# Kernel tuning notes

Hardware: AMD Instinct MI355X
Metric: run time of the kernel (lower is better)

The kernel has to match this reference:

```python
import jax, jax.numpy as jnp
import numpy as np

B, NK, NQ = 16, 1024, 1024
D_IN, D_V, D_H = 3, 8, 128
NUGGET = 1e-3   # diagonal regularizer for the kriging covariance solve
EPS = 1e-12     # keeps sqrt differentiable at zero distance


def _mlp(x, w1, b1, w2, b2, w3, b3):
    # Linear -> ReLU -> Linear -> ReLU -> Linear (torch Linear: y = x @ W.T + b)
    h = jax.nn.relu(x @ w1.T + b1)
    h = jax.nn.relu(h @ w2.T + b2)
    return h @ w3.T + b3


def _cdist(a, b):
    # a: [B,N,D], b: [B,M,D] -> [B,N,M] Euclidean distances
    d2 = (jnp.sum(a * a, -1)[:, :, None]
          + jnp.sum(b * b, -1)[:, None, :]
          - 2.0 * jnp.einsum('bnd,bmd->bnm', a, b))
    return jnp.sqrt(jnp.maximum(d2, 0.0) + EPS)


def _linear_init(key, out_f, in_f):
    k1, k2 = jax.random.split(key)
    lim = 1.0 / np.sqrt(in_f)
    w = jax.random.uniform(k1, (out_f, in_f), jnp.float32, -lim, lim)
    b = jax.random.uniform(k2, (out_f,), jnp.float32, -lim, lim)
    return w, b


def setup_inputs() -> dict:
    key = jax.random.key(0)
    ks = jax.random.split(key, 10)
    KEY = jax.random.normal(ks[0], (B, NK, D_IN), jnp.float32)
    VALUE = jax.random.normal(ks[1], (B, NK, D_V), jnp.float32)
    QUERY = jax.random.normal(ks[2], (B, NQ, D_IN), jnp.float32)
    W1_w, W1_b = _linear_init(ks[3], D_H, D_IN)
    W2_w, W2_b = _linear_init(ks[4], D_H, D_H)
    W3_w, W3_b = _linear_init(ks[5], D_IN, D_H)
    Wv1_w, Wv1_b = _linear_init(ks[6], D_H, D_V)
    Wv2_w, Wv2_b = _linear_init(ks[7], D_H, D_H)
    Wv3_w, Wv3_b = _linear_init(ks[8], D_V, D_H)
    return dict(KEY=KEY, VALUE=VALUE, QUERY=QUERY,
                W1_w=W1_w, W1_b=W1_b, W2_w=W2_w, W2_b=W2_b, W3_w=W3_w, W3_b=W3_b,
                Wv1_w=Wv1_w, Wv1_b=Wv1_b, Wv2_w=Wv2_w, Wv2_b=Wv2_b, Wv3_w=Wv3_w, Wv3_b=Wv3_b)


def reference(KEY, VALUE, QUERY,
              W1_w, W1_b, W2_w, W2_b, W3_w, W3_b,
              Wv1_w, Wv1_b, Wv2_w, Wv2_b, Wv3_w, Wv3_b):
    # shared MLP on KEY and QUERY, separate MLP on VALUE
    Wk = _mlp(KEY, W1_w, W1_b, W2_w, W2_b, W3_w, W3_b)
    Wq = _mlp(QUERY, W1_w, W1_b, W2_w, W2_b, W3_w, W3_b)
    Wv = _mlp(VALUE, Wv1_w, Wv1_b, Wv2_w, Wv2_b, Wv3_w, Wv3_b)
    VALUE_scale = VALUE * Wv                  # einsum('bij,bij->bij')
    # kriging prediction with learned elementwise coordinate scalings
    Ks = KEY * Wk                             # [B,NK,D_IN]
    Qs = QUERY * Wq                           # [B,NQ,D_IN]
    C_kk = jnp.exp(-_cdist(Ks, Ks)) + NUGGET * jnp.eye(NK, dtype=KEY.dtype)  # [B,NK,NK]
    C_qk = jnp.exp(-_cdist(Qs, Ks))                                          # [B,NQ,NK]
    # kriging weights: solve C_kk @ lam = C_qk^T  -> lam [B,NK,NQ]
    lam = jnp.linalg.solve(C_kk, jnp.swapaxes(C_qk, 1, 2))
    # prediction: weighted sum of scaled values -> [B,NQ,D_V]
    return jnp.einsum('bkq,bkv->bqv', lam, VALUE_scale)
```

## Files before the change

### kernel.cpp

```cpp
#include <hip/hip_runtime.h>
#include <hip/hip_bf16.h>


__device__ __forceinline__ int row_of(int e) {
    int i = (int)((sqrtf(8.0f * (float)e + 1.0f) - 1.0f) * 0.5f);
    while ((i + 1) * (i + 2) / 2 <= e) i++;
    while (i * (i + 1) / 2 > e) i--;
    return i;
}

__global__ void k_transpose(const float* __restrict__ W2, const float* __restrict__ Wv2,
                            float* __restrict__ W2T, float* __restrict__ Wv2T) {
    int tid = blockIdx.x * 256 + threadIdx.x;
    int e = tid & 16383;
    int r = e >> 7, c = e & 127;
    if (tid < 16384) W2T[c * 128 + r] = W2[e];
    else             Wv2T[c * 128 + r] = Wv2[e];
}

template<int DI, int P>
__device__ __forceinline__ void mlp_body(const float* __restrict__ in,
                                         float* __restrict__ out, int base,
                                         const float* __restrict__ W1,
                                         const float* __restrict__ b1,
                                         const float* __restrict__ W2T,
                                         const float* __restrict__ b2,
                                         const float* __restrict__ W3,
                                         const float* __restrict__ b3) {
    __shared__ float xs[P][DI];
    __shared__ float h1[P][128];
    __shared__ float h2[P][129];
    int t = threadIdx.x;
    for (int i = t; i < P * DI; i += 128) xs[i / DI][i % DI] = in[base * DI + i];
    __syncthreads();
    float w1r[DI];
#pragma unroll
    for (int d = 0; d < DI; d++) w1r[d] = W1[t * DI + d];
    float b1t = b1[t], b2t = b2[t];
#pragma unroll
    for (int p = 0; p < P; p++) {
        float s = b1t;
#pragma unroll
        for (int d = 0; d < DI; d++) s += w1r[d] * xs[p][d];
        h1[p][t] = fmaxf(s, 0.0f);
    }
    __syncthreads();
    float acc[P];
#pragma unroll
    for (int p = 0; p < P; p++) acc[p] = b2t;
    for (int k = 0; k < 128; k++) {
        float w = W2T[k * 128 + t];
#pragma unroll
        for (int p = 0; p < P; p++) acc[p] += w * h1[p][k];
    }
#pragma unroll
    for (int p = 0; p < P; p++) h2[p][t] = fmaxf(acc[p], 0.0f);
    __syncthreads();
    if (t < P * DI) {
        int p = t / DI, d = t % DI;
        float s = b3[d];
        for (int k = 0; k < 128; k++) s += W3[d * 128 + k] * h2[p][k];
        int gi = base * DI + t;
        out[gi] = in[gi] * s;
    }
}

__global__ void k_mlp_kq(const float* __restrict__ KEY, float* __restrict__ Ks,
                         const float* __restrict__ QUERY, float* __restrict__ Qs,
                         const float* __restrict__ W1, const float* __restrict__ b1,
                         const float* __restrict__ W2T, const float* __restrict__ b2,
                         const float* __restrict__ W3, const float* __restrict__ b3) {
    if (blockIdx.x < 512)
        mlp_body<3, 32>(KEY, Ks, blockIdx.x * 32, W1, b1, W2T, b2, W3, b3);
    else
        mlp_body<3, 32>(QUERY, Qs, (blockIdx.x - 512) * 32, W1, b1, W2T, b2, W3, b3);
}

__global__ void k_mlp_v(const float* __restrict__ VALUE, float* __restrict__ Vs,
                        const float* __restrict__ W1, const float* __restrict__ b1,
                        const float* __restrict__ W2T, const float* __restrict__ b2,
                        const float* __restrict__ W3, const float* __restrict__ b3) {
    mlp_body<8, 16>(VALUE, Vs, blockIdx.x * 16, W1, b1, W2T, b2, W3, b3);
}

__global__ void k_buildC(const float* __restrict__ Ks, float* __restrict__ C) {
    long idx = (long)blockIdx.x * 256 + threadIdx.x;
    int b = (int)(idx >> 20);
    int rem = (int)(idx & 1048575);
    int i = rem >> 10, j = rem & 1023;
    const float* a = Ks + ((long)b * 1024 + i) * 3;
    const float* bb = Ks + ((long)b * 1024 + j) * 3;
    float d0 = a[0] - bb[0], d1 = a[1] - bb[1], d2 = a[2] - bb[2];
    float dist = sqrtf(d0 * d0 + d1 * d1 + d2 * d2 + 1e-12f);
    float v = __expf(-dist);
    if (i == j) v += 1e-3f;
    C[idx] = v;
}

__device__ void potf_body(float* __restrict__ C, float* __restrict__ V,
                          int o, int last, int b) {
    int tid = threadIdx.x;
    float* A = C + (long)b * 1048576;
    float* Vp = V + (long)b * 8192;
    __shared__ float T[128][132];
    __shared__ __align__(16) float cv[128][8];
    __shared__ __align__(16) float cw[128][8];
    __shared__ __align__(16) float Pn[128][8];
    __shared__ __align__(16) float St[32][132];
    __shared__ float rsd[128];
    __shared__ float W[32][33];
    __shared__ float zs[128][9];
    bool active = (tid < 136);
    int ti = 0, tj = 0;
    if (active) { ti = row_of(tid); tj = tid - ti * (ti + 1) / 2; }
    int r0 = ti * 8, c0t = tj * 8;
    float Treg[8][8];
    if (active) {
        const float* src = A + (long)(o + r0) * 1024 + o + c0t;
#pragma unroll
        for (int i = 0; i < 8; i++) {
            float4 va = *(const float4*)(src + (long)i * 1024);
            float4 vb = *(const float4*)(src + (long)i * 1024 + 4);
            Treg[i][0] = va.x; Treg[i][1] = va.y; Treg[i][2] = va.z; Treg[i][3] = va.w;
            Treg[i][4] = vb.x; Treg[i][5] = vb.y; Treg[i][6] = vb.z; Treg[i][7] = vb.w;
        }
    }
    int lane = tid & 63;
    __syncthreads();
    if (o > 0) {
        for (int kc = 0; kc < 4; kc++) {
            {
                int r = tid >> 1, lk = (tid & 1) * 16;
                const float* sp = A + (long)(o + r) * 1024 + (o - 128) + kc * 32 + lk;
#pragma unroll
                for (int k4 = 0; k4 < 4; k4++) {
                    float4 v = *(const float4*)(sp + 4 * k4);
                    St[lk + 4*k4    ][r] = v.x;
                    St[lk + 4*k4 + 1][r] = v.y;
                    St[lk + 4*k4 + 2][r] = v.z;
                    St[lk + 4*k4 + 3][r] = v.w;
                }
            }
            __syncthreads();
            if (active) {
#pragma unroll 4
                for (int k = 0; k < 32; k++) {
                    float4 a0 = *(const float4*)&St[k][r0];
                    float4 a1 = *(const float4*)&St[k][r0 + 4];
                    float4 b0 = *(const float4*)&St[k][c0t];
                    float4 b1 = *(const float4*)&St[k][c0t + 4];
                    float aa[8] = {a0.x,a0.y,a0.z,a0.w,a1.x,a1.y,a1.z,a1.w};
                    float bb[8] = {b0.x,b0.y,b0.z,b0.w,b1.x,b1.y,b1.z,b1.w};
#pragma unroll
                    for (int i = 0; i < 8; i++)
#pragma unroll
                        for (int j = 0; j < 8; j++) Treg[i][j] -= aa[i] * bb[j];
                }
            }
            __syncthreads();
        }
    }
    for (int jbt = 0; jbt < 16; jbt++) {
        int jb = jbt * 8;
        if (active && tj == jbt) {
#pragma unroll
            for (int i = 0; i < 8; i++) {
                *(float4*)&Pn[r0 + i][0] = make_float4(Treg[i][0], Treg[i][1], Treg[i][2], Treg[i][3]);
                *(float4*)&Pn[r0 + i][4] = make_float4(Treg[i][4], Treg[i][5], Treg[i][6], Treg[i][7]);
            }
        }
        __syncthreads();
        if (tid < 64) {
            int r1 = lane, r2 = 64 + lane;
            float v1[8], v2[8], w1[8], w2[8];
#pragma unroll
            for (int q = 0; q < 8; q++) {
                int j = jb + q;
                int jl = j & 63;
                bool hi = (j >= 64);
                float a1 = Pn[r1][q], a2 = Pn[r2][q];
#pragma unroll
                for (int p = 0; p < 8; p++) {
                    if (p < q) {
                        float wj = __shfl(hi ? w2[p] : w1[p], jl);
                        a1 -= v1[p] * wj;
                        a2 -= v2[p] * wj;
                    }
                }
                v1[q] = a1; v2[q] = a2;
                float dj = __shfl(hi ? a2 : a1, jl);
                float dinv = 1.0f / dj;
                w1[q] = a1 * dinv; w2[q] = a2 * dinv;
            }
            *(float4*)&cv[r1][0] = make_float4(v1[0], v1[1], v1[2], v1[3]);
            *(float4*)&cv[r1][4] = make_float4(v1[4], v1[5], v1[6], v1[7]);
            *(float4*)&cv[r2][0] = make_float4(v2[0], v2[1], v2[2], v2[3]);
            *(float4*)&cv[r2][4] = make_float4(v2[4], v2[5], v2[6], v2[7]);
            *(float4*)&cw[r1][0] = make_float4(w1[0], w1[1], w1[2], w1[3]);
            *(float4*)&cw[r1][4] = make_float4(w1[4], w1[5], w1[6], w1[7]);
            *(float4*)&cw[r2][0] = make_float4(w2[0], w2[1], w2[2], w2[3]);
            *(float4*)&cw[r2][4] = make_float4(w2[4], w2[5], w2[6], w2[7]);
        }
        __syncthreads();
        if (active && tj == jbt) {
#pragma unroll
            for (int i = 0; i < 8; i++) {
                float4 va = *(const float4*)&cv[r0 + i][0];
                float4 vb = *(const float4*)&cv[r0 + i][4];
                Treg[i][0] = va.x; Treg[i][1] = va.y; Treg[i][2] = va.z; Treg[i][3] = va.w;
                Treg[i][4] = vb.x; Treg[i][5] = vb.y; Treg[i][6] = vb.z; Treg[i][7] = vb.w;
            }
        } else if (active && tj > jbt) {
#pragma unroll
            for (int h = 0; h < 2; h++) {
                float va4[8][4], wb4[8][4];
#pragma unroll
                for (int i = 0; i < 8; i++) {
                    float4 v = *(const float4*)&cv[r0 + i][h * 4];
                    va4[i][0] = v.x; va4[i][1] = v.y; va4[i][2] = v.z; va4[i][3] = v.w;
                }
#pragma unroll
                for (int j = 0; j < 8; j++) {
                    float4 v = *(const float4*)&cw[c0t + j][h * 4];
                    wb4[j][0] = v.x; wb4[j][1] = v.y; wb4[j][2] = v.z; wb4[j][3] = v.w;
                }
#pragma unroll
                for (int i = 0; i < 8; i++)
#pragma unroll
                    for (int j = 0; j < 8; j++)
                        Treg[i][j] -= va4[i][0] * wb4[j][0] + va4[i][1] * wb4[j][1]
                                    + va4[i][2] * wb4[j][2] + va4[i][3] * wb4[j][3];
            }
        }
        __syncthreads();
    }
    if (active) {
#pragma unroll
        for (int i = 0; i < 8; i++) {
            *(float4*)&T[r0 + i][c0t]     = make_float4(Treg[i][0], Treg[i][1], Treg[i][2], Treg[i][3]);
            *(float4*)&T[r0 + i][c0t + 4] = make_float4(Treg[i][4], Treg[i][5], Treg[i][6], Treg[i][7]);
        }
    }
    __syncthreads();
    int rg = tid >> 4;
    int cg = tid & 15;
    int wv = tid >> 6;
    if (tid < 128) rsd[tid] = rsqrtf(T[tid][tid]);
    __syncthreads();
#pragma unroll
    for (int j = 0; j < 8; j++) {
        int c = cg + 16 * j;
#pragma unroll
        for (int i = 0; i < 8; i++) {
            int r = rg * 8 + i;
            if (c <= r) T[r][c] *= rsd[c];
            else        T[r][c] = 0.0f;
        }
    }
    __syncthreads();
    if (lane < 32) {
        int d0 = wv * 32;
        int j = lane;
        float x[32];
#pragma unroll
        for (int i = 0; i < 32; i++) {
            float dinv = 1.0f / T[d0 + i][d0 + i];
            float s = 0.0f;
#pragma unroll
            for (int k = 0; k < i; k++) s += T[d0 + i][d0 + k] * x[k];
            x[i] = (i == j) ? dinv : -s * dinv;
        }
#pragma unroll
        for (int i = 0; i < 32; i++) T[d0 + i][d0 + j] = x[i];
    }
    __syncthreads();
    int orr = tid >> 3;
    int oc = (tid & 7) * 4;
    for (int j = 0; j < 3; j++) {
        for (int i = j + 1; i < 4; i++) {
            float w0 = 0, w1 = 0, w2 = 0, w3 = 0;
            for (int kb = j; kb < i; kb++) {
#pragma unroll 8
                for (int kk = 0; kk < 32; kk++) {
                    float l = T[i * 32 + orr][kb * 32 + kk];
                    w0 += l * T[kb * 32 + kk][j * 32 + oc    ];
                    w1 += l * T[kb * 32 + kk][j * 32 + oc + 1];
                    w2 += l * T[kb * 32 + kk][j * 32 + oc + 2];
                    w3 += l * T[kb * 32 + kk][j * 32 + oc + 3];
                }
            }
            W[orr][oc] = w0; W[orr][oc+1] = w1; W[orr][oc+2] = w2; W[orr][oc+3] = w3;
            __syncthreads();
            float v0 = 0, v1 = 0, v2 = 0, v3 = 0;
#pragma unroll 8
            for (int kk = 0; kk < 32; kk++) {
                float l = T[i * 32 + orr][i * 32 + kk];
                v0 += l * W[kk][oc    ];
                v1 += l * W[kk][oc + 1];
                v2 += l * W[kk][oc + 2];
                v3 += l * W[kk][oc + 3];
            }
            __syncthreads();
            T[i * 32 + orr][j * 32 + oc    ] = -v0;
            T[i * 32 + orr][j * 32 + oc + 1] = -v1;
            T[i * 32 + orr][j * 32 + oc + 2] = -v2;
            T[i * 32 + orr][j * 32 + oc + 3] = -v3;
            __syncthreads();
        }
    }
    {
        int r = tid >> 1, c0 = (tid & 1) * 64;
        float* dst = A + (long)(o + r) * 1024 + o + c0;
#pragma unroll
        for (int k = 0; k < 16; k++) {
            int c = c0 + 4 * k;
            float4 v = make_float4(T[r][c], T[r][c + 1], T[r][c + 2], T[r][c + 3]);
            *(float4*)(dst + 4 * k) = v;
        }
    }
    {
        int k = tid >> 1, c0 = (tid & 1) * 4;
        float4 v = *(const float4*)&Vp[(o + k) * 8 + c0];
        zs[k][c0] = v.x; zs[k][c0 + 1] = v.y; zs[k][c0 + 2] = v.z; zs[k][c0 + 3] = v.w;
    }
    __syncthreads();
    {
        int r = tid & 127, c0 = (tid >> 7) * 4;
        float y0 = 0, y1 = 0, y2 = 0, y3 = 0;
#pragma unroll 8
        for (int k = 0; k < 128; k++) {
            float l = T[r][k];
            y0 += l * zs[k][c0    ];
            y1 += l * zs[k][c0 + 1];
            y2 += l * zs[k][c0 + 2];
            y3 += l * zs[k][c0 + 3];
        }
        if (!last) {
            *(float4*)&Vp[(o + r) * 8 + c0] = make_float4(y0, y1, y2, y3);
        } else {
            __syncthreads();
            zs[r][c0] = y0; zs[r][c0+1] = y1; zs[r][c0+2] = y2; zs[r][c0+3] = y3;
            __syncthreads();
            float x0 = 0, x1 = 0, x2 = 0, x3 = 0;
#pragma unroll 8
            for (int k = 0; k < 128; k++) {
                float l = T[k][r];
                x0 += l * zs[k][c0    ];
                x1 += l * zs[k][c0 + 1];
                x2 += l * zs[k][c0 + 2];
                x3 += l * zs[k][c0 + 3];
            }
            *(float4*)&Vp[(o + r) * 8 + c0] = make_float4(x0, x1, x2, x3);
        }
    }
}

__device__ void syrk_body(float* __restrict__ C, int o, int pti, int ptj, int b) {
    float* A = C + (long)b * 1048576;
    int bi = o + 128 + pti * 128, bj = o + 128 + ptj * 128;
    __shared__ float As[32][132];
    __shared__ float Bs[32][132];
    int tid = threadIdx.x;
    int tx = tid & 15, ty = tid >> 4;
    float acc[8][8] = {};
    int lr = tid >> 1;
    int lk = (tid & 1) * 16;
    bool diag = (bi == bj);
    for (int kc = 0; kc < 128; kc += 32) {
        {
            const float* src = A + (long)(bi + lr) * 1024 + o + kc + lk;
#pragma unroll
            for (int k4 = 0; k4 < 4; k4++) {
                float4 v = *(const float4*)(src + 4 * k4);
                As[lk + 4*k4    ][lr] = v.x;
                As[lk + 4*k4 + 1][lr] = v.y;
                As[lk + 4*k4 + 2][lr] = v.z;
                As[lk + 4*k4 + 3][lr] = v.w;
            }
            if (!diag) {
                const float* sb = A + (long)(bj + lr) * 1024 + o + kc + lk;
#pragma unroll
                for (int k4 = 0; k4 < 4; k4++) {
                    float4 v = *(const float4*)(sb + 4 * k4);
                    Bs[lk + 4*k4    ][lr] = v.x;
                    Bs[lk + 4*k4 + 1][lr] = v.y;
                    Bs[lk + 4*k4 + 2][lr] = v.z;
                    Bs[lk + 4*k4 + 3][lr] = v.w;
                }
            }
        }
        __syncthreads();
        {
            const float (*Bp)[132] = diag ? As : Bs;
#pragma unroll
            for (int k = 0; k < 32; k++) {
                float4 a0 = *(const float4*)&As[k][ty * 8];
                float4 a1 = *(const float4*)&As[k][ty * 8 + 4];
                float4 b0 = *(const float4*)&Bp[k][tx * 8];
                float4 b1 = *(const float4*)&Bp[k][tx * 8 + 4];
                float aa[8] = {a0.x,a0.y,a0.z,a0.w,a1.x,a1.y,a1.z,a1.w};
                float bb[8] = {b0.x,b0.y,b0.z,b0.w,b1.x,b1.y,b1.z,b1.w};
#pragma unroll
                for (int i = 0; i < 8; i++)
#pragma unroll
                    for (int j = 0; j < 8; j++) acc[i][j] += aa[i] * bb[j];
            }
        }
        __syncthreads();
    }
#pragma unroll
    for (int i = 0; i < 8; i++) {
        int r = bi + ty * 8 + i;
        float* dst = A + (long)r * 1024 + bj + tx * 8;
        if (!diag) {
            float4 p0 = *(const float4*)dst;
            float4 p1 = *(const float4*)(dst + 4);
            p0.x -= acc[i][0]; p0.y -= acc[i][1]; p0.z -= acc[i][2]; p0.w -= acc[i][3];
            p1.x -= acc[i][4]; p1.y -= acc[i][5]; p1.z -= acc[i][6]; p1.w -= acc[i][7];
            *(float4*)dst = p0;
            *(float4*)(dst + 4) = p1;
        } else {
#pragma unroll
            for (int j = 0; j < 8; j++) {
                int c = bj + tx * 8 + j;
                if (c <= r) dst[j] -= acc[i][j];
            }
        }
    }
}

__global__ __launch_bounds__(256) void k_potf_syrk(float* __restrict__ C,
                                                   float* __restrict__ V,
                                                   int o, int last) {
    int bx = blockIdx.x;
    if (bx < 16) {
        potf_body(C, V, o, last, bx);
    } else {
        int v = bx - 16;
        int bb = v & 15;
        int p = (v >> 4) + 1;
        int tii = row_of(p);
        int tjj = p - tii * (tii + 1) / 2;
        syrk_body(C, o - 128, tii, tjj, bb);
    }
}

__global__ __launch_bounds__(256) void k_trsmg(float* __restrict__ C,
                                               float* __restrict__ V, int o) {
    int b = blockIdx.y;
    float* A = C + (long)b * 1048576;
    float* Vp = V + (long)b * 8192;
    int bi = o + 128 + blockIdx.x * 128;
    const float* Linv = A + (long)o * 1024 + o;
    __shared__ float As[32][132];
    __shared__ float Ls[32][132];
    int tid = threadIdx.x;
    int tx = tid & 15, ty = tid >> 4;
    float acc[8][8] = {};
    int lr = tid >> 1;
    int lk = (tid & 1) * 16;
    for (int kc = 0; kc < 128; kc += 32) {
        const float* src = A + (long)(bi + lr) * 1024 + o + kc + lk;
        const float* sl  = Linv + (long)lr * 1024 + kc + lk;
#pragma unroll
        for (int k4 = 0; k4 < 4; k4++) {
            float4 v = *(const float4*)(src + 4 * k4);
            As[lk + 4*k4    ][lr] = v.x;
            As[lk + 4*k4 + 1][lr] = v.y;
            As[lk + 4*k4 + 2][lr] = v.z;
            As[lk + 4*k4 + 3][lr] = v.w;
            float4 w = *(const float4*)(sl + 4 * k4);
            Ls[lk + 4*k4    ][lr] = w.x;
            Ls[lk + 4*k4 + 1][lr] = w.y;
            Ls[lk + 4*k4 + 2][lr] = w.z;
            Ls[lk + 4*k4 + 3][lr] = w.w;
        }
        __syncthreads();
#pragma unroll
        for (int k = 0; k < 32; k++) {
            float4 a0 = *(const float4*)&As[k][ty * 8];
            float4 a1 = *(const float4*)&As[k][ty * 8 + 4];
            float4 b0 = *(const float4*)&Ls[k][tx * 8];
            float4 b1 = *(const float4*)&Ls[k][tx * 8 + 4];
            float aa[8] = {a0.x,a0.y,a0.z,a0.w,a1.x,a1.y,a1.z,a1.w};
            float bb[8] = {b0.x,b0.y,b0.z,b0.w,b1.x,b1.y,b1.z,b1.w};
#pragma unroll
            for (int i = 0; i < 8; i++)
#pragma unroll
                for (int j = 0; j < 8; j++) acc[i][j] += aa[i] * bb[j];
        }
        __syncthreads();
    }
#pragma unroll
    for (int i = 0; i < 8; i++) {
        float* dst = A + (long)(bi + ty * 8 + i) * 1024 + o + tx * 8;
        *(float4*)dst       = make_float4(acc[i][0], acc[i][1], acc[i][2], acc[i][3]);
        *(float4*)(dst + 4) = make_float4(acc[i][4], acc[i][5], acc[i][6], acc[i][7]);
    }
    float* ysf = &Ls[0][0];
    {
        int k = tid >> 1, c0 = (tid & 1) * 4;
        float4 v = *(const float4*)&Vp[(o + k) * 8 + c0];
        ysf[k * 9 + c0] = v.x; ysf[k * 9 + c0 + 1] = v.y;
        ysf[k * 9 + c0 + 2] = v.z; ysf[k * 9 + c0 + 3] = v.w;
    }
    __syncthreads();
    float zacc0 = 0, zacc1 = 0, zacc2 = 0, zacc3 = 0;
    int zr = tid & 127, zc0 = (tid >> 7) * 4;
#pragma unroll
    for (int ch = 0; ch < 4; ch++) {
        if ((tx >> 2) == ch) {
            int cb = (tx & 3) * 8;
#pragma unroll
            for (int j = 0; j < 8; j++)
#pragma unroll
                for (int i = 0; i < 8; i++)
                    As[cb + j][ty * 8 + i] = acc[i][j];
        }
        __syncthreads();
#pragma unroll 8
        for (int k = 0; k < 32; k++) {
            float l = As[k][zr];
            const float* yp = &ysf[(ch * 32 + k) * 9 + zc0];
            zacc0 += l * yp[0]; zacc1 += l * yp[1];
            zacc2 += l * yp[2]; zacc3 += l * yp[3];
        }
        __syncthreads();
    }
    float* vp = &Vp[(bi + zr) * 8 + zc0];
    float4 old = *(const float4*)vp;
    old.x -= zacc0; old.y -= zacc1; old.z -= zacc2; old.w -= zacc3;
    *(float4*)vp = old;
}

__global__ __launch_bounds__(256) void k_bstep(const float* __restrict__ C,
                                               float* __restrict__ V, int k) {
    int b = blockIdx.y, j = blockIdx.x, tid = threadIdx.x;
    const float* A = C + (long)b * 1048576;
    float* Vp = V + (long)b * 8192;
    __shared__ float Lb[128][129];
    __shared__ float xs[128][9];
    __shared__ float ys[128][9];
    {
        int kk = tid >> 1, c0 = (tid & 1) * 4;
        float4 v = *(const float4*)&Vp[(k * 128 + kk) * 8 + c0];
        xs[kk][c0] = v.x; xs[kk][c0+1] = v.y; xs[kk][c0+2] = v.z; xs[kk][c0+3] = v.w;
    }
#pragma unroll
    for (int m = 0; m < 16; m++) {
        int e = tid + m * 256;
        int i = e >> 5, j4 = (e & 31) * 4;
        float4 v = *(const float4*)&A[(long)(k * 128 + i) * 1024 + j * 128 + j4];
        Lb[i][j4] = v.x; Lb[i][j4+1] = v.y; Lb[i][j4+2] = v.z; Lb[i][j4+3] = v.w;
    }
    __syncthreads();
    int r = tid & 127, c0 = (tid >> 7) * 4;
    float u0 = 0, u1 = 0, u2 = 0, u3 = 0;
#pragma unroll 8
    for (int kk = 0; kk < 128; kk++) {
        float l = Lb[kk][r];
        u0 += l * xs[kk][c0    ];
        u1 += l * xs[kk][c0 + 1];
        u2 += l * xs[kk][c0 + 2];
        u3 += l * xs[kk][c0 + 3];
    }
    float* vp = &Vp[(j * 128 + r) * 8 + c0];
    float4 old = *(const float4*)vp;
    old.x -= u0; old.y -= u1; old.z -= u2; old.w -= u3;
    if (j < k - 1) {
        *(float4*)vp = old;
    } else {
        ys[r][c0] = old.x; ys[r][c0+1] = old.y; ys[r][c0+2] = old.z; ys[r][c0+3] = old.w;
        __syncthreads();
        int o = j * 128;
#pragma unroll
        for (int m = 0; m < 16; m++) {
            int e = tid + m * 256;
            int i = e >> 5, j4 = (e & 31) * 4;
            float4 v = *(const float4*)&A[(long)(o + i) * 1024 + o + j4];
            Lb[i][j4] = v.x; Lb[i][j4+1] = v.y; Lb[i][j4+2] = v.z; Lb[i][j4+3] = v.w;
        }
        __syncthreads();
        float x0 = 0, x1 = 0, x2 = 0, x3 = 0;
#pragma unroll 8
        for (int kk = 0; kk < 128; kk++) {
            float l = Lb[kk][r];
            x0 += l * ys[kk][c0    ];
            x1 += l * ys[kk][c0 + 1];
            x2 += l * ys[kk][c0 + 2];
            x3 += l * ys[kk][c0 + 3];
        }
        *(float4*)vp = make_float4(x0, x1, x2, x3);
    }
}

__global__ void k_out(const float* __restrict__ Qs, const float* __restrict__ Ks,
                      const float* __restrict__ X, float* __restrict__ out) {
    int b = blockIdx.x >> 4;
    int qc = blockIdx.x & 15;
    int t = threadIdx.x;
    int q = t & 63, ks = t >> 6;
    __shared__ float kx[1024][3];
    __shared__ __align__(16) float xv[1024][8];
    __shared__ float red[4][64][8];
    for (int i = t; i < 3072; i += 256) kx[i / 3][i % 3] = Ks[b * 3072 + i];
    for (int i = t; i < 8192; i += 256) xv[i >> 3][i & 7] = X[b * 8192 + i];
    __syncthreads();
    int gq = b * 1024 + qc * 64 + q;
    const float* qp = Qs + (long)gq * 3;
    float qx = qp[0], qy = qp[1], qz = qp[2];
    float acc[8] = {};
    int k0 = ks * 256;
#pragma unroll 2
    for (int k = k0; k < k0 + 256; k++) {
        float dx = qx - kx[k][0], dy = qy - kx[k][1], dz = qz - kx[k][2];
        float w = __expf(-sqrtf(dx * dx + dy * dy + dz * dz + 1e-12f));
        float4 xa = *(const float4*)&xv[k][0];
        float4 xb = *(const float4*)&xv[k][4];
        acc[0] += w * xa.x; acc[1] += w * xa.y; acc[2] += w * xa.z; acc[3] += w * xa.w;
        acc[4] += w * xb.x; acc[5] += w * xb.y; acc[6] += w * xb.z; acc[7] += w * xb.w;
    }
#pragma unroll
    for (int c = 0; c < 8; c++) red[ks][q][c] = acc[c];
    __syncthreads();
    if (ks == 0) {
        float* op = out + (long)gq * 8;
#pragma unroll
        for (int c = 0; c < 8; c++)
            op[c] = red[0][q][c] + red[1][q][c] + red[2][q][c] + red[3][q][c];
    }
}

extern "C" void kernel_launch(void* const* d_in, const int* in_sizes, int n_in,
                              void* d_out, int out_size, void* d_ws, size_t ws_size,
                              hipStream_t stream) {
    const float* KEY   = (const float*)d_in[0];
    const float* VALUE = (const float*)d_in[1];
    const float* QUERY = (const float*)d_in[2];
    const float* W1w = (const float*)d_in[3];  const float* W1b = (const float*)d_in[4];
    const float* W2w = (const float*)d_in[5];  const float* W2b = (const float*)d_in[6];
    const float* W3w = (const float*)d_in[7];  const float* W3b = (const float*)d_in[8];
    const float* Wv1w = (const float*)d_in[9]; const float* Wv1b = (const float*)d_in[10];
    const float* Wv2w = (const float*)d_in[11];const float* Wv2b = (const float*)d_in[12];
    const float* Wv3w = (const float*)d_in[13];const float* Wv3b = (const float*)d_in[14];

    float* ws  = (float*)d_ws;
    float* C    = ws;
    float* Ks   = C + 16777216;
    float* Qs   = Ks + 49152;
    float* Vs   = Qs + 49152;
    float* W2T  = Vs + 131072;
    float* Wv2T = W2T + 16384;

    float* out = (float*)d_out;

    hipLaunchKernelGGL(k_transpose, dim3(128), dim3(256), 0, stream, W2w, Wv2w, W2T, Wv2T);
    hipLaunchKernelGGL(k_mlp_kq, dim3(1024), dim3(128), 0, stream,
                       KEY, Ks, QUERY, Qs, W1w, W1b, W2T, W2b, W3w, W3b);
    hipLaunchKernelGGL(k_mlp_v, dim3(1024), dim3(128), 0, stream,
                       VALUE, Vs, Wv1w, Wv1b, Wv2T, Wv2b, Wv3w, Wv3b);
    hipLaunchKernelGGL(k_buildC, dim3(65536), dim3(256), 0, stream, Ks, C);

    for (int s = 0; s < 8; s++) {
        int o = s * 128;
        int np = 0;
        if (s >= 1) { int ntp = 8 - s; np = ntp * (ntp + 1) / 2 - 1; }
        hipLaunchKernelGGL(k_potf_syrk, dim3(16 + np * 16), dim3(256), 0, stream,
                           C, Vs, o, (s == 7) ? 1 : 0);
        int nt = 7 - s;
        if (nt > 0)
            hipLaunchKernelGGL(k_trsmg, dim3(nt, 16), dim3(256), 0, stream, C, Vs, o);
    }
    for (int k = 7; k >= 1; k--)
        hipLaunchKernelGGL(k_bstep, dim3(k, 16), dim3(256), 0, stream, C, Vs, k);

    hipLaunchKernelGGL(k_out, dim3(256), dim3(256), 0, stream, Qs, Ks, Vs, out);
}
```

Measured before the change: 1.140 ms.

## Fuse blocked Cholesky and solve steps into one persistent kernel with per-batch barriers

```diff
diff --git a/kernel.cpp b/kernel.cpp
--- a/kernel.cpp
+++ b/kernel.cpp
@@ -9,9 +9,37 @@
     return i;
 }
 
+struct PotfS {
+    float T[128][132];
+    float cv[128][8];
+    float cw[128][8];
+    float Pn[128][8];
+    float St[32][132];
+    float rsd[128];
+    float W[32][33];
+    float zs[128][9];
+};
+struct SyrkS { float As[32][132]; float Bs[32][132]; };
+struct TrsmS { float As[32][132]; float Ls[32][132]; };
+struct BstepS { float Lb[128][129]; float xs[128][9]; float ys[128][9]; };
+#define SMEM_BYTES 106112
+
+__device__ __forceinline__ void batch_barrier(unsigned int* cnt) {
+    __syncthreads();
+    if (threadIdx.x == 0) {
+        __threadfence();
+        atomicAdd(cnt, 1u);
+        while (atomicAdd(cnt, 0u) < 16u) __builtin_amdgcn_s_sleep(1);
+    }
+    __syncthreads();
+    __threadfence();
+}
+
 __global__ void k_transpose(const float* __restrict__ W2, const float* __restrict__ Wv2,
-                            float* __restrict__ W2T, float* __restrict__ Wv2T) {
+                            float* __restrict__ W2T, float* __restrict__ Wv2T,
+                            unsigned int* __restrict__ bar) {
     int tid = blockIdx.x * 256 + threadIdx.x;
+    if (tid < 512) bar[tid] = 0u;
     int e = tid & 16383;
     int r = e >> 7, c = e & 127;
     if (tid < 16384) W2T[c * 128 + r] = W2[e];
@@ -98,18 +126,19 @@
 }
 
 __device__ void potf_body(float* __restrict__ C, float* __restrict__ V,
-                          int o, int last, int b) {
+                          int o, int last, int b, char* smem) {
+    PotfS& S = *(PotfS*)smem;
+    float (&T)[128][132] = S.T;
+    float (&cv)[128][8] = S.cv;
+    float (&cw)[128][8] = S.cw;
+    float (&Pn)[128][8] = S.Pn;
+    float (&St)[32][132] = S.St;
+    float (&rsd)[128] = S.rsd;
+    float (&W)[32][33] = S.W;
+    float (&zs)[128][9] = S.zs;
     int tid = threadIdx.x;
     float* A = C + (long)b * 1048576;
     float* Vp = V + (long)b * 8192;
-    __shared__ float T[128][132];
-    __shared__ __align__(16) float cv[128][8];
-    __shared__ __align__(16) float cw[128][8];
-    __shared__ __align__(16) float Pn[128][8];
-    __shared__ __align__(16) float St[32][132];
-    __shared__ float rsd[128];
-    __shared__ float W[32][33];
-    __shared__ float zs[128][9];
     bool active = (tid < 136);
     int ti = 0, tj = 0;
     if (active) { ti = row_of(tid); tj = tid - ti * (ti + 1) / 2; }
@@ -355,17 +384,20 @@
     }
 }
 
-__device__ void syrk_body(float* __restrict__ C, int o, int pti, int ptj, int b) {
+__device__ void syrk_body(float* __restrict__ C, int o, int pti, int ptj, int b,
+                          char* smem) {
+    SyrkS& S = *(SyrkS*)smem;
+    float (&As)[32][132] = S.As;
+    float (&Bs)[32][132] = S.Bs;
     float* A = C + (long)b * 1048576;
     int bi = o + 128 + pti * 128, bj = o + 128 + ptj * 128;
-    __shared__ float As[32][132];
-    __shared__ float Bs[32][132];
     int tid = threadIdx.x;
     int tx = tid & 15, ty = tid >> 4;
     float acc[8][8] = {};
     int lr = tid >> 1;
     int lk = (tid & 1) * 16;
     bool diag = (bi == bj);
+    __syncthreads();
     for (int kc = 0; kc < 128; kc += 32) {
         {
             const float* src = A + (long)(bi + lr) * 1024 + o + kc + lk;
@@ -429,36 +461,21 @@
     }
 }
 
-__global__ __launch_bounds__(256) void k_potf_syrk(float* __restrict__ C,
-                                                   float* __restrict__ V,
-                                                   int o, int last) {
-    int bx = blockIdx.x;
-    if (bx < 16) {
-        potf_body(C, V, o, last, bx);
-    } else {
-        int v = bx - 16;
-        int bb = v & 15;
-        int p = (v >> 4) + 1;
-        int tii = row_of(p);
-        int tjj = p - tii * (tii + 1) / 2;
-        syrk_body(C, o - 128, tii, tjj, bb);
-    }
-}
-
-__global__ __launch_bounds__(256) void k_trsmg(float* __restrict__ C,
-                                               float* __restrict__ V, int o) {
-    int b = blockIdx.y;
+__device__ void trsmg_body(float* __restrict__ C, float* __restrict__ V,
+                           int o, int rowblk, int b, char* smem) {
+    TrsmS& S = *(TrsmS*)smem;
+    float (&As)[32][132] = S.As;
+    float (&Ls)[32][132] = S.Ls;
     float* A = C + (long)b * 1048576;
     float* Vp = V + (long)b * 8192;
-    int bi = o + 128 + blockIdx.x * 128;
+    int bi = o + 128 + rowblk * 128;
     const float* Linv = A + (long)o * 1024 + o;
-    __shared__ float As[32][132];
-    __shared__ float Ls[32][132];
     int tid = threadIdx.x;
     int tx = tid & 15, ty = tid >> 4;
     float acc[8][8] = {};
     int lr = tid >> 1;
     int lk = (tid & 1) * 16;
+    __syncthreads();
     for (int kc = 0; kc < 128; kc += 32) {
         const float* src = A + (long)(bi + lr) * 1024 + o + kc + lk;
         const float* sl  = Linv + (long)lr * 1024 + kc + lk;
@@ -533,14 +550,16 @@
     *(float4*)vp = old;
 }
 
-__global__ __launch_bounds__(256) void k_bstep(const float* __restrict__ C,
-                                               float* __restrict__ V, int k) {
-    int b = blockIdx.y, j = blockIdx.x, tid = threadIdx.x;
+__device__ void bstep_body(const float* __restrict__ C, float* __restrict__ V,
+                           int k, int j, int b, char* smem) {
+    BstepS& S = *(BstepS*)smem;
+    float (&Lb)[128][129] = S.Lb;
+    float (&xs)[128][9] = S.xs;
+    float (&ys)[128][9] = S.ys;
     const float* A = C + (long)b * 1048576;
     float* Vp = V + (long)b * 8192;
-    __shared__ float Lb[128][129];
-    __shared__ float xs[128][9];
-    __shared__ float ys[128][9];
+    int tid = threadIdx.x;
+    __syncthreads();
     {
         int kk = tid >> 1, c0 = (tid & 1) * 4;
         float4 v = *(const float4*)&Vp[(k * 128 + kk) * 8 + c0];
@@ -591,6 +610,40 @@
             x3 += l * ys[kk][c0 + 3];
         }
         *(float4*)vp = make_float4(x0, x1, x2, x3);
+    }
+}
+
+__global__ __launch_bounds__(256) void k_chol(float* __restrict__ C,
+                                              float* __restrict__ V,
+                                              unsigned int* __restrict__ bar) {
+    __shared__ __align__(16) char smem[SMEM_BYTES];
+    int b = blockIdx.x & 15;
+    int role = blockIdx.x >> 4;
+    unsigned int* cnt = bar + b * 32;
+    int slot = 0;
+    for (int s = 0; s < 8; s++) {
+        int o = s * 128;
+        if (role == 0) {
+            potf_body(C, V, o, (s == 7) ? 1 : 0, b, smem);
+        } else if (s >= 1) {
+            int ntp = 8 - s;
+            int npt = ntp * (ntp + 1) / 2;
+            for (int p = role; p < npt; p += 15) {
+                int tii = row_of(p);
+                int tjj = p - tii * (tii + 1) / 2;
+                syrk_body(C, o - 128, tii, tjj, b, smem);
+            }
+        }
+        batch_barrier(cnt + slot); slot++;
+        int nt = 7 - s;
+        if (nt > 0) {
+            if (role < nt) trsmg_body(C, V, o, role, b, smem);
+            batch_barrier(cnt + slot); slot++;
+        }
+    }
+    for (int k = 7; k >= 1; k--) {
+        if (role < k) bstep_body(C, V, k, role, b, smem);
+        batch_barrier(cnt + slot); slot++;
     }
 }
 
@@ -651,28 +704,19 @@
     float* Vs   = Qs + 49152;
     float* W2T  = Vs + 131072;
     float* Wv2T = W2T + 16384;
+    unsigned int* bar = (unsigned int*)(Wv2T + 16384);
 
     float* out = (float*)d_out;
 
-    hipLaunchKernelGGL(k_transpose, dim3(128), dim3(256), 0, stream, W2w, Wv2w, W2T, Wv2T);
+    hipLaunchKernelGGL(k_transpose, dim3(128), dim3(256), 0, stream,
+                       W2w, Wv2w, W2T, Wv2T, bar);
     hipLaunchKernelGGL(k_mlp_kq, dim3(1024), dim3(128), 0, stream,
                        KEY, Ks, QUERY, Qs, W1w, W1b, W2T, W2b, W3w, W3b);
     hipLaunchKernelGGL(k_mlp_v, dim3(1024), dim3(128), 0, stream,
                        VALUE, Vs, Wv1w, Wv1b, Wv2T, Wv2b, Wv3w, Wv3b);
     hipLaunchKernelGGL(k_buildC, dim3(65536), dim3(256), 0, stream, Ks, C);
 
-    for (int s = 0; s < 8; s++) {
-        int o = s * 128;
-        int np = 0;
-        if (s >= 1) { int ntp = 8 - s; np = ntp * (ntp + 1) / 2 - 1; }
-        hipLaunchKernelGGL(k_potf_syrk, dim3(16 + np * 16), dim3(256), 0, stream,
-                           C, Vs, o, (s == 7) ? 1 : 0);
-        int nt = 7 - s;
-        if (nt > 0)
-            hipLaunchKernelGGL(k_trsmg, dim3(nt, 16), dim3(256), 0, stream, C, Vs, o);
-    }
-    for (int k = 7; k >= 1; k--)
-        hipLaunchKernelGGL(k_bstep, dim3(k, 16), dim3(256), 0, stream, C, Vs, k);
+    hipLaunchKernelGGL(k_chol, dim3(256), dim3(256), 0, stream, C, Vs, bar);
 
     hipLaunchKernelGGL(k_out, dim3(256), dim3(256), 0, stream, Qs, Ks, Vs, out);
 }
```

Measured after the change: 1.580 ms. 38.6% more time.

## Merge MLP kernels and vectorize diagonal-block inverse with transposed LDS buffers

Applied to the files above, without the earlier changes.

```diff
diff --git a/kernel.cpp b/kernel.cpp
--- a/kernel.cpp
+++ b/kernel.cpp
@@ -65,22 +65,21 @@
     }
 }
 
-__global__ void k_mlp_kq(const float* __restrict__ KEY, float* __restrict__ Ks,
-                         const float* __restrict__ QUERY, float* __restrict__ Qs,
-                         const float* __restrict__ W1, const float* __restrict__ b1,
-                         const float* __restrict__ W2T, const float* __restrict__ b2,
-                         const float* __restrict__ W3, const float* __restrict__ b3) {
+__global__ void k_mlp_all(const float* __restrict__ KEY, float* __restrict__ Ks,
+                          const float* __restrict__ QUERY, float* __restrict__ Qs,
+                          const float* __restrict__ VALUE, float* __restrict__ Vs,
+                          const float* __restrict__ W1, const float* __restrict__ b1,
+                          const float* __restrict__ W2T, const float* __restrict__ b2,
+                          const float* __restrict__ W3, const float* __restrict__ b3,
+                          const float* __restrict__ Wv1, const float* __restrict__ bv1,
+                          const float* __restrict__ Wv2T, const float* __restrict__ bv2,
+                          const float* __restrict__ Wv3, const float* __restrict__ bv3) {
     if (blockIdx.x < 512)
         mlp_body<3, 32>(KEY, Ks, blockIdx.x * 32, W1, b1, W2T, b2, W3, b3);
+    else if (blockIdx.x < 1024)
+        mlp_body<3, 32>(QUERY, Qs, (blockIdx.x - 512) * 32, W1, b1, W2T, b2, W3, b3);
     else
-        mlp_body<3, 32>(QUERY, Qs, (blockIdx.x - 512) * 32, W1, b1, W2T, b2, W3, b3);
-}
-
-__global__ void k_mlp_v(const float* __restrict__ VALUE, float* __restrict__ Vs,
-                        const float* __restrict__ W1, const float* __restrict__ b1,
-                        const float* __restrict__ W2T, const float* __restrict__ b2,
-                        const float* __restrict__ W3, const float* __restrict__ b3) {
-    mlp_body<8, 16>(VALUE, Vs, blockIdx.x * 16, W1, b1, W2T, b2, W3, b3);
+        mlp_body<8, 16>(VALUE, Vs, (blockIdx.x - 1024) * 16, Wv1, bv1, Wv2T, bv2, Wv3, bv3);
 }
 
 __global__ void k_buildC(const float* __restrict__ Ks, float* __restrict__ C) {
@@ -103,13 +102,16 @@
     float* A = C + (long)b * 1048576;
     float* Vp = V + (long)b * 8192;
     __shared__ float T[128][132];
-    __shared__ __align__(16) float cv[128][8];
-    __shared__ __align__(16) float cw[128][8];
-    __shared__ __align__(16) float Pn[128][8];
-    __shared__ __align__(16) float St[32][132];
+    __shared__ __align__(16) char arena[29184];
     __shared__ float rsd[128];
-    __shared__ float W[32][33];
-    __shared__ float zs[128][9];
+    __shared__ __align__(16) float WT[32][36];
+    __shared__ __align__(16) float zsT[8][132];
+    float (*cv)[8]  = (float(*)[8])(arena);
+    float (*cw)[8]  = (float(*)[8])(arena + 4096);
+    float (*Pn)[8]  = (float(*)[8])(arena + 8192);
+    float (*St)[132] = (float(*)[132])(arena + 12288);
+    typedef float XTrow[32][36];
+    XTrow* XT = (XTrow*)arena;
     bool active = (tid < 136);
     int ti = 0, tj = 0;
     if (active) { ti = row_of(tid); tj = tid - ti * (ti + 1) / 2; }
@@ -274,38 +276,70 @@
         for (int i = 0; i < 32; i++) T[d0 + i][d0 + j] = x[i];
     }
     __syncthreads();
-    int orr = tid >> 3;
-    int oc = (tid & 7) * 4;
-    for (int j = 0; j < 3; j++) {
-        for (int i = j + 1; i < 4; i++) {
-            float w0 = 0, w1 = 0, w2 = 0, w3 = 0;
-            for (int kb = j; kb < i; kb++) {
-#pragma unroll 8
-                for (int kk = 0; kk < 32; kk++) {
-                    float l = T[i * 32 + orr][kb * 32 + kk];
-                    w0 += l * T[kb * 32 + kk][j * 32 + oc    ];
-                    w1 += l * T[kb * 32 + kk][j * 32 + oc + 1];
-                    w2 += l * T[kb * 32 + kk][j * 32 + oc + 2];
-                    w3 += l * T[kb * 32 + kk][j * 32 + oc + 3];
-                }
-            }
-            W[orr][oc] = w0; W[orr][oc+1] = w1; W[orr][oc+2] = w2; W[orr][oc+3] = w3;
+    {
+        int orr = tid >> 3;
+        int oc0 = tid & 7;
+        for (int j = 0; j < 3; j++) {
+#pragma unroll
+            for (int m = 0; m < 4; m++) {
+                int e = tid + 256 * m;
+                int c = e >> 5, r = e & 31;
+                XT[j][c][r] = T[j * 32 + r][j * 32 + c];
+            }
             __syncthreads();
-            float v0 = 0, v1 = 0, v2 = 0, v3 = 0;
-#pragma unroll 8
-            for (int kk = 0; kk < 32; kk++) {
-                float l = T[i * 32 + orr][i * 32 + kk];
-                v0 += l * W[kk][oc    ];
-                v1 += l * W[kk][oc + 1];
-                v2 += l * W[kk][oc + 2];
-                v3 += l * W[kk][oc + 3];
-            }
-            __syncthreads();
-            T[i * 32 + orr][j * 32 + oc    ] = -v0;
-            T[i * 32 + orr][j * 32 + oc + 1] = -v1;
-            T[i * 32 + orr][j * 32 + oc + 2] = -v2;
-            T[i * 32 + orr][j * 32 + oc + 3] = -v3;
-            __syncthreads();
+            for (int i = j + 1; i < 4; i++) {
+                float w_[4] = {0, 0, 0, 0};
+                for (int kb = j; kb < i; kb++) {
+                    const float4* tr = (const float4*)&T[i * 32 + orr][kb * 32];
+                    float4 t0 = tr[0], t1 = tr[1], t2 = tr[2], t3 = tr[3];
+                    float4 t4 = tr[4], t5 = tr[5], t6 = tr[6], t7 = tr[7];
+#pragma unroll
+                    for (int m = 0; m < 4; m++) {
+                        const float4* xr = (const float4*)&XT[kb][oc0 + 8 * m][0];
+                        float s = 0.0f;
+                        float4 a;
+                        a = xr[0]; s += t0.x*a.x + t0.y*a.y + t0.z*a.z + t0.w*a.w;
+                        a = xr[1]; s += t1.x*a.x + t1.y*a.y + t1.z*a.z + t1.w*a.w;
+                        a = xr[2]; s += t2.x*a.x + t2.y*a.y + t2.z*a.z + t2.w*a.w;
+                        a = xr[3]; s += t3.x*a.x + t3.y*a.y + t3.z*a.z + t3.w*a.w;
+                        a = xr[4]; s += t4.x*a.x + t4.y*a.y + t4.z*a.z + t4.w*a.w;
+                        a = xr[5]; s += t5.x*a.x + t5.y*a.y + t5.z*a.z + t5.w*a.w;
+                        a = xr[6]; s += t6.x*a.x + t6.y*a.y + t6.z*a.z + t6.w*a.w;
+                        a = xr[7]; s += t7.x*a.x + t7.y*a.y + t7.z*a.z + t7.w*a.w;
+                        w_[m] += s;
+                    }
+                }
+#pragma unroll
+                for (int m = 0; m < 4; m++) WT[oc0 + 8 * m][orr] = w_[m];
+                __syncthreads();
+                float v_[4];
+                {
+                    const float4* lr4 = (const float4*)&T[i * 32 + orr][i * 32];
+                    float4 t0 = lr4[0], t1 = lr4[1], t2 = lr4[2], t3 = lr4[3];
+                    float4 t4 = lr4[4], t5 = lr4[5], t6 = lr4[6], t7 = lr4[7];
+#pragma unroll
+                    for (int m = 0; m < 4; m++) {
+                        const float4* wr = (const float4*)&WT[oc0 + 8 * m][0];
+                        float s = 0.0f;
+                        float4 a;
+                        a = wr[0]; s += t0.x*a.x + t0.y*a.y + t0.z*a.z + t0.w*a.w;
+                        a = wr[1]; s += t1.x*a.x + t1.y*a.y + t1.z*a.z + t1.w*a.w;
+                        a = wr[2]; s += t2.x*a.x + t2.y*a.y + t2.z*a.z + t2.w*a.w;
+                        a = wr[3]; s += t3.x*a.x + t3.y*a.y + t3.z*a.z + t3.w*a.w;
+                        a = wr[4]; s += t4.x*a.x + t4.y*a.y + t4.z*a.z + t4.w*a.w;
+                        a = wr[5]; s += t5.x*a.x + t5.y*a.y + t5.z*a.z + t5.w*a.w;
+                        a = wr[6]; s += t6.x*a.x + t6.y*a.y + t6.z*a.z + t6.w*a.w;
+                        a = wr[7]; s += t7.x*a.x + t7.y*a.y + t7.z*a.z + t7.w*a.w;
+                        v_[m] = s;
+                    }
+                }
+#pragma unroll
+                for (int m = 0; m < 4; m++) {
+                    T[i * 32 + orr][j * 32 + oc0 + 8 * m] = -v_[m];
+                    XT[i][oc0 + 8 * m][orr] = -v_[m];
+                }
+                __syncthreads();
+            }
         }
     }
     {
@@ -321,34 +355,44 @@
     {
         int k = tid >> 1, c0 = (tid & 1) * 4;
         float4 v = *(const float4*)&Vp[(o + k) * 8 + c0];
-        zs[k][c0] = v.x; zs[k][c0 + 1] = v.y; zs[k][c0 + 2] = v.z; zs[k][c0 + 3] = v.w;
+        zsT[c0][k] = v.x; zsT[c0 + 1][k] = v.y; zsT[c0 + 2][k] = v.z; zsT[c0 + 3][k] = v.w;
     }
     __syncthreads();
     {
         int r = tid & 127, c0 = (tid >> 7) * 4;
+        const float4* trow = (const float4*)&T[r][0];
+        const float4* z0 = (const float4*)&zsT[c0][0];
+        const float4* z1 = (const float4*)&zsT[c0 + 1][0];
+        const float4* z2 = (const float4*)&zsT[c0 + 2][0];
+        const float4* z3 = (const float4*)&zsT[c0 + 3][0];
         float y0 = 0, y1 = 0, y2 = 0, y3 = 0;
 #pragma unroll 8
-        for (int k = 0; k < 128; k++) {
-            float l = T[r][k];
-            y0 += l * zs[k][c0    ];
-            y1 += l * zs[k][c0 + 1];
-            y2 += l * zs[k][c0 + 2];
-            y3 += l * zs[k][c0 + 3];
+        for (int q = 0; q < 32; q++) {
+            float4 t = trow[q];
+            float4 a0 = z0[q], a1 = z1[q], a2 = z2[q], a3 = z3[q];
+            y0 += t.x*a0.x + t.y*a0.y + t.z*a0.z + t.w*a0.w;
+            y1 += t.x*a1.x + t.y*a1.y + t.z*a1.z + t.w*a1.w;
+            y2 += t.x*a2.x + t.y*a2.y + t.z*a2.z + t.w*a2.w;
+            y3 += t.x*a3.x + t.y*a3.y + t.z*a3.z + t.w*a3.w;
         }
         if (!last) {
             *(float4*)&Vp[(o + r) * 8 + c0] = make_float4(y0, y1, y2, y3);
         } else {
             __syncthreads();
-            zs[r][c0] = y0; zs[r][c0+1] = y1; zs[r][c0+2] = y2; zs[r][c0+3] = y3;
+            zsT[c0][r] = y0; zsT[c0+1][r] = y1; zsT[c0+2][r] = y2; zsT[c0+3][r] = y3;
             __syncthreads();
             float x0 = 0, x1 = 0, x2 = 0, x3 = 0;
-#pragma unroll 8
-            for (int k = 0; k < 128; k++) {
-                float l = T[k][r];
-                x0 += l * zs[k][c0    ];
-                x1 += l * zs[k][c0 + 1];
-                x2 += l * zs[k][c0 + 2];
-                x3 += l * zs[k][c0 + 3];
+#pragma unroll 4
+            for (int q = 0; q < 32; q++) {
+                float l0 = T[4*q    ][r];
+                float l1 = T[4*q + 1][r];
+                float l2 = T[4*q + 2][r];
+                float l3 = T[4*q + 3][r];
+                float4 a0 = z0[q], a1 = z1[q], a2 = z2[q], a3 = z3[q];
+                x0 += l0*a0.x + l1*a0.y + l2*a0.z + l3*a0.w;
+                x1 += l0*a1.x + l1*a1.y + l2*a1.z + l3*a1.w;
+                x2 += l0*a2.x + l1*a2.y + l2*a2.z + l3*a2.w;
+                x3 += l0*a3.x + l1*a3.y + l2*a3.z + l3*a3.w;
             }
             *(float4*)&Vp[(o + r) * 8 + c0] = make_float4(x0, x1, x2, x3);
         }
@@ -655,10 +699,10 @@
     float* out = (float*)d_out;
 
     hipLaunchKernelGGL(k_transpose, dim3(128), dim3(256), 0, stream, W2w, Wv2w, W2T, Wv2T);
-    hipLaunchKernelGGL(k_mlp_kq, dim3(1024), dim3(128), 0, stream,
-                       KEY, Ks, QUERY, Qs, W1w, W1b, W2T, W2b, W3w, W3b);
-    hipLaunchKernelGGL(k_mlp_v, dim3(1024), dim3(128), 0, stream,
-                       VALUE, Vs, Wv1w, Wv1b, Wv2T, Wv2b, Wv3w, Wv3b);
+    hipLaunchKernelGGL(k_mlp_all, dim3(2048), dim3(128), 0, stream,
+                       KEY, Ks, QUERY, Qs, VALUE, Vs,
+                       W1w, W1b, W2T, W2b, W3w, W3b,
+                       Wv1w, Wv1b, Wv2T, Wv2b, Wv3w, Wv3b);
     hipLaunchKernelGGL(k_buildC, dim3(65536), dim3(256), 0, stream, Ks, C);
 
     for (int s = 0; s < 8; s++) {
```

Result: slower. 1.163 ms (+2.0%).
